# Optimization experiments

Measured on AMD Instinct MI355X. Metric: run time of the kernel, lower is better.

Reference implementation:

```python
import math
import jax, jax.numpy as jnp
import numpy as np

B, T, D, N = 4, 4096, 2048, 512
FACIL_RATE = 2.0
FIRE_THRESH = 0.85
MAX_GATE = 8.0
EPS = 1e-12  # F.normalize eps


def _gelu(x):
    c = math.sqrt(2.0 / math.pi)
    return 0.5 * x * (1.0 + jnp.tanh(c * (x + 0.044715 * x ** 3)))


def _normalize(v, axis=-1):
    n = jnp.linalg.norm(v, axis=axis, keepdims=True)
    return v / jnp.maximum(n, EPS)


def setup_inputs() -> dict:
    key = jax.random.key(0)
    k1, k2, k3 = jax.random.split(key, 3)
    return {
        "x": jax.random.normal(k1, (B, T, D), dtype=jnp.float32),
        "log_k_mag": jnp.asarray(math.log(0.5), dtype=jnp.float32),
        "keys": jax.random.normal(k2, (N, D), dtype=jnp.float32),
        "mag": jax.random.uniform(k3, (N, D), dtype=jnp.float32, minval=0.1, maxval=1.0),
        "facil": jnp.full((N,), 2.0, dtype=jnp.float32),
        "mask": jnp.ones((N,), dtype=bool),
    }


def reference(x, log_k_mag, keys, mag, facil, mask):
    Bb, Tt, Dd = x.shape
    k_mag = jnp.clip(jnp.exp(log_k_mag), 0.01, 5.0)
    y = _gelu(x)  # [B,T,D]
    # torch detaches y before the buffer math
    y_flat = jax.lax.stop_gradient(y.reshape(Bb * Tt, Dd))
    y_mean = y_flat.mean(0)  # [D]
    m_n = _normalize(y_mean, axis=0)
    keys_n = _normalize(keys)  # [N,D]
    sims = jnp.where(mask, keys_n @ m_n, -1.0)  # [N]
    idx = jnp.argmax(sims)
    fire = sims[idx] > FIRE_THRESH
    facil_level = jnp.where(fire, facil[idx] * FACIL_RATE, facil[idx])
    mag_vec = mag[idx]  # [D]
    importance = mag_vec / jnp.maximum(mag_vec.mean(), 1e-6)
    mv_n = keys_n[idx]  # [D] (already L2-normalized key)
    y_n = _normalize(y_flat)  # [B*T, D]
    tok_sim = jnp.clip(y_n @ mv_n, 0.0, 1.0).reshape(Bb, Tt, 1)
    gate_d = jnp.minimum(1.0 + k_mag * (facil_level - 1.0) * importance, MAX_GATE)  # [D]
    gate = gate_d.reshape(1, 1, Dd) * tok_sim + (1.0 - tok_sim)
    return y * gate
```

## Files before the change

kernel.cpp:

```cpp
#include <hip/hip_runtime.h>
#include <math.h>

#define ROWS 16384
#define D    2048
#define NKEYS 512
#define NCHUNK 1024
#define CROWS (ROWS / NCHUNK)
#define NPANEL 8
#define PCOLS (D / NPANEL)

__device__ inline float gelu1(float v) {
    float t = 0.7978845608028654f * fmaf(0.044715f * v, v * v, v);
    float e = __expf(2.0f * t);
    return v * (1.0f - 1.0f / (e + 1.0f));
}

__device__ inline float4 gelu4(float4 v) {
    float4 r;
    r.x = gelu1(v.x); r.y = gelu1(v.y); r.z = gelu1(v.z); r.w = gelu1(v.w);
    return r;
}

__device__ inline void acc4(float4& a, float4 v) {
    a.x += v.x; a.y += v.y; a.z += v.z; a.w += v.w;
}

__device__ inline void block_reduce_sum2(float& a, float& b) {
    __shared__ float sa[4], sb[4];
    for (int off = 32; off; off >>= 1) {
        a += __shfl_down(a, off, 64);
        b += __shfl_down(b, off, 64);
    }
    const int lane = threadIdx.x & 63, w = threadIdx.x >> 6;
    if (lane == 0) { sa[w] = a; sb[w] = b; }
    __syncthreads();
    if (threadIdx.x == 0) {
        a = sa[0] + sa[1] + sa[2] + sa[3];
        b = sb[0] + sb[1] + sb[2] + sb[3];
        sa[0] = a; sb[0] = b;
    }
    __syncthreads();
    a = sa[0]; b = sb[0];
    __syncthreads();
}

__global__ __launch_bounds__(256) void colsum_kernel(const float* __restrict__ x,
                                                     float* __restrict__ partials) {
    const int rc = blockIdx.x >> 3;
    const int p  = blockIdx.x & 7;
    const int t  = threadIdx.x;
    const int w    = t >> 6;
    const int lane = t & 63;

    const size_t base = (size_t)(rc * CROWS + w) * (D / 4) + p * (PCOLS / 4) + lane;
    const float4* x4 = (const float4*)x;
    float4 l0 = x4[base + 0 * 4 * (D / 4)];
    float4 l1 = x4[base + 1 * 4 * (D / 4)];
    float4 l2 = x4[base + 2 * 4 * (D / 4)];
    float4 l3 = x4[base + 3 * 4 * (D / 4)];

    float4 a = gelu4(l0);
    acc4(a, gelu4(l1));
    acc4(a, gelu4(l2));
    acc4(a, gelu4(l3));

    __shared__ float4 sm[4][64];
    sm[w][lane] = a;
    __syncthreads();
    if (t < 64) {
        float4 s = sm[0][t];
        acc4(s, sm[1][t]);
        acc4(s, sm[2][t]);
        acc4(s, sm[3][t]);
        float4* pr = (float4*)(partials + (size_t)rc * D + p * PCOLS);
        pr[t] = s;
    }
}

__global__ __launch_bounds__(256) void reduce_kernel(const float* __restrict__ partials,
                                                     float* __restrict__ colsum) {
    const int t = threadIdx.x;
    const int cidx = t & 15;
    const int rg   = t >> 4;
    const int c = blockIdx.x * 16 + cidx;
    float s = 0.f;
    #pragma unroll 8
    for (int r = rg; r < NCHUNK; r += 16) {
        s += partials[(size_t)r * D + c];
    }
    __shared__ float sm[256];
    sm[t] = s;
    __syncthreads();
    if (t < 16) {
        float acc = 0.f;
        #pragma unroll
        for (int k = 0; k < 16; ++k) acc += sm[t + 16 * k];
        colsum[blockIdx.x * 16 + t] = acc;
    }
}

__global__ __launch_bounds__(256) void sims_kernel(const float* __restrict__ keys,
                                                   const float* __restrict__ colsum,
                                                   float* __restrict__ sims) {
    const int i = blockIdx.x;
    const int t = threadIdx.x;
    const float4* kr = (const float4*)(keys + (size_t)i * D);
    const float4* s4 = (const float4*)colsum;
    float4 k0 = kr[t], k1 = kr[t + 256];
    float4 c0 = s4[t], c1 = s4[t + 256];
    float dot = k0.x*c0.x + k0.y*c0.y + k0.z*c0.z + k0.w*c0.w
              + k1.x*c1.x + k1.y*c1.y + k1.z*c1.z + k1.w*c1.w;
    float ksq = k0.x*k0.x + k0.y*k0.y + k0.z*k0.z + k0.w*k0.w
              + k1.x*k1.x + k1.y*k1.y + k1.z*k1.z + k1.w*k1.w;
    block_reduce_sum2(dot, ksq);
    if (t == 0) sims[i] = dot / fmaxf(sqrtf(ksq), 1e-12f);
}

__global__ __launch_bounds__(256) void finalize_kernel(const float* __restrict__ colsum,
                                                       const float* __restrict__ sims,
                                                       const float* __restrict__ keys,
                                                       const float* __restrict__ mag,
                                                       const float* __restrict__ facil,
                                                       const float* __restrict__ logk,
                                                       float* __restrict__ gate_d,
                                                       float* __restrict__ mv_n) {
    const int t = threadIdx.x;
    __shared__ float sv[256];
    __shared__ int   si[256];
    __shared__ int   s_idx;
    __shared__ float s_val;

    float best = -3.402823466e38f; int bidx = 0;
    for (int i = t; i < NKEYS; i += 256) {
        float v = sims[i];
        if (v > best) { best = v; bidx = i; }
    }
    sv[t] = best; si[t] = bidx;
    __syncthreads();
    if (t == 0) {
        float bv = sv[0]; int bi = si[0];
        for (int i = 1; i < 256; i++) {
            if (sv[i] > bv || (sv[i] == bv && si[i] < bi)) { bv = sv[i]; bi = si[i]; }
        }
        s_idx = bi; s_val = bv;
    }
    __syncthreads();
    const int idx = s_idx;

    float ss = 0.f, dummy = 0.f;
    for (int d = t; d < D; d += 256) { float v = colsum[d]; ss += v * v; }
    block_reduce_sum2(ss, dummy);
    const float normS = fmaxf(sqrtf(ss), 1e-12f);
    const float true_sim = s_val / normS;
    const bool fire = true_sim > 0.85f;

    const float fl = facil[idx] * (fire ? 2.0f : 1.0f);
    const float km = fminf(fmaxf(expf(logk[0]), 0.01f), 5.0f);

    const float4* mrow4 = (const float4*)(mag  + (size_t)idx * D);
    const float4* krow4 = (const float4*)(keys + (size_t)idx * D);
    float4 mA = mrow4[t], mB = mrow4[t + 256];
    float4 kA = krow4[t], kB = krow4[t + 256];
    float msum = mA.x + mA.y + mA.z + mA.w + mB.x + mB.y + mB.z + mB.w;
    float ksq  = kA.x*kA.x + kA.y*kA.y + kA.z*kA.z + kA.w*kA.w
               + kB.x*kB.x + kB.y*kB.y + kB.z*kB.z + kB.w*kB.w;
    block_reduce_sum2(msum, ksq);
    const float mmean = fmaxf(msum / (float)D, 1e-6f);
    const float knorm = fmaxf(sqrtf(ksq), 1e-12f);
    const float coef = km * (fl - 1.0f) / mmean;
    const float rkn = 1.0f / knorm;

    float4 gA, gB, nA, nB;
    gA.x = fminf(fmaf(coef, mA.x, 1.0f), 8.0f);
    gA.y = fminf(fmaf(coef, mA.y, 1.0f), 8.0f);
    gA.z = fminf(fmaf(coef, mA.z, 1.0f), 8.0f);
    gA.w = fminf(fmaf(coef, mA.w, 1.0f), 8.0f);
    gB.x = fminf(fmaf(coef, mB.x, 1.0f), 8.0f);
    gB.y = fminf(fmaf(coef, mB.y, 1.0f), 8.0f);
    gB.z = fminf(fmaf(coef, mB.z, 1.0f), 8.0f);
    gB.w = fminf(fmaf(coef, mB.w, 1.0f), 8.0f);
    nA.x = kA.x * rkn; nA.y = kA.y * rkn; nA.z = kA.z * rkn; nA.w = kA.w * rkn;
    nB.x = kB.x * rkn; nB.y = kB.y * rkn; nB.z = kB.z * rkn; nB.w = kB.w * rkn;

    float4* g4 = (float4*)gate_d;
    float4* n4 = (float4*)mv_n;
    g4[t]       = gA;
    g4[t + 256] = gB;
    n4[t]       = nA;
    n4[t + 256] = nB;
}

__global__ __launch_bounds__(256) void main_kernel(const float* __restrict__ x,
                                                   const float* __restrict__ gate_d,
                                                   const float* __restrict__ mv_n,
                                                   float* __restrict__ out) {
    const int w    = threadIdx.x >> 6;
    const int lane = threadIdx.x & 63;
    const int row  = blockIdx.x * 4 + w;

    const float4* xr  = (const float4*)(x + (size_t)row * D) + lane;
    const float4* mv4 = (const float4*)mv_n + lane;

    float4 xv[8];
    #pragma unroll
    for (int i = 0; i < 8; ++i) xv[i] = xr[i * 64];

    float4 y[8];
    float dot = 0.f, ss = 0.f;
    #pragma unroll
    for (int i = 0; i < 8; ++i) {
        y[i] = gelu4(xv[i]);
        float4 m = mv4[i * 64];
        dot += y[i].x*m.x + y[i].y*m.y + y[i].z*m.z + y[i].w*m.w;
        ss  += y[i].x*y[i].x + y[i].y*y[i].y + y[i].z*y[i].z + y[i].w*y[i].w;
    }

    #pragma unroll
    for (int off = 32; off; off >>= 1) {
        dot += __shfl_xor(dot, off, 64);
        ss  += __shfl_xor(ss,  off, 64);
    }

    float ts = dot / fmaxf(sqrtf(ss), 1e-12f);
    ts = fminf(fmaxf(ts, 0.0f), 1.0f);
    const float omts = 1.0f - ts;

    const float4* g4 = (const float4*)gate_d + lane;
    float4* o4 = (float4*)(out + (size_t)row * D) + lane;
    #pragma unroll
    for (int i = 0; i < 8; ++i) {
        float4 g = g4[i * 64];
        float4 o;
        o.x = y[i].x * fmaf(g.x, ts, omts);
        o.y = y[i].y * fmaf(g.y, ts, omts);
        o.z = y[i].z * fmaf(g.z, ts, omts);
        o.w = y[i].w * fmaf(g.w, ts, omts);
        o4[i * 64] = o;
    }
}

extern "C" void kernel_launch(void* const* d_in, const int* in_sizes, int n_in,
                              void* d_out, int out_size, void* d_ws, size_t ws_size,
                              hipStream_t stream) {
    const float* x     = (const float*)d_in[0];
    const float* logk  = (const float*)d_in[1];
    const float* keys  = (const float*)d_in[2];
    const float* mag   = (const float*)d_in[3];
    const float* facil = (const float*)d_in[4];
    float* out = (float*)d_out;

    float* ws       = (float*)d_ws;
    float* colsum   = ws;
    float* sims     = ws + 2048;
    float* gate_d   = ws + 2560;
    float* mv_n     = ws + 4608;
    float* partials = ws + 6656;

    colsum_kernel  <<<NCHUNK * NPANEL, 256, 0, stream>>>(x, partials);
    reduce_kernel  <<<D / 16, 256, 0, stream>>>(partials, colsum);
    sims_kernel    <<<NKEYS, 256, 0, stream>>>(keys, colsum, sims);
    finalize_kernel<<<1, 256, 0, stream>>>(colsum, sims, keys, mag, facil, logk, gate_d, mv_n);
    main_kernel    <<<ROWS / 4, 256, 0, stream>>>(x, gate_d, mv_n, out);
}
```

Baseline: 104.2 us.

## Cache GELU output as fp16 in first pass and reuse it in apply

The first pass now computes GELU once, writes it as fp16 to workspace, and accumulates column partials over 16-row blocks. The apply kernel reads the fp16 activations instead of recomputing GELU from fp32 input, and uses nontemporal loads and stores. This trades a full fp32 re-read plus GELU recompute for an fp16 write and read, at the cost of output precision.

```diff
diff --git a/kernel.cpp b/kernel.cpp
--- a/kernel.cpp
+++ b/kernel.cpp
@@ -5,9 +5,10 @@
 #define D    2048
 #define NKEYS 512
 #define NCHUNK 1024
-#define CROWS (ROWS / NCHUNK)
-#define NPANEL 8
-#define PCOLS (D / NPANEL)
+
+typedef float    fvec4 __attribute__((ext_vector_type(4)));
+typedef _Float16 half4 __attribute__((ext_vector_type(4)));
+typedef _Float16 half8 __attribute__((ext_vector_type(8)));
 
 __device__ inline float gelu1(float v) {
     float t = 0.7978845608028654f * fmaf(0.044715f * v, v * v, v);
@@ -16,6 +17,11 @@
 }
 
 __device__ inline float4 gelu4(float4 v) {
+    float4 r;
+    r.x = gelu1(v.x); r.y = gelu1(v.y); r.z = gelu1(v.z); r.w = gelu1(v.w);
+    return r;
+}
+__device__ inline float4 gelu4(fvec4 v) {
     float4 r;
     r.x = gelu1(v.x); r.y = gelu1(v.y); r.z = gelu1(v.z); r.w = gelu1(v.w);
     return r;
@@ -44,37 +50,51 @@
     __syncthreads();
 }
 
-__global__ __launch_bounds__(256) void colsum_kernel(const float* __restrict__ x,
-                                                     float* __restrict__ partials) {
-    const int rc = blockIdx.x >> 3;
-    const int p  = blockIdx.x & 7;
-    const int t  = threadIdx.x;
-    const int w    = t >> 6;
-    const int lane = t & 63;
-
-    const size_t base = (size_t)(rc * CROWS + w) * (D / 4) + p * (PCOLS / 4) + lane;
-    const float4* x4 = (const float4*)x;
-    float4 l0 = x4[base + 0 * 4 * (D / 4)];
-    float4 l1 = x4[base + 1 * 4 * (D / 4)];
-    float4 l2 = x4[base + 2 * 4 * (D / 4)];
-    float4 l3 = x4[base + 3 * 4 * (D / 4)];
-
-    float4 a = gelu4(l0);
-    acc4(a, gelu4(l1));
-    acc4(a, gelu4(l2));
-    acc4(a, gelu4(l3));
-
-    __shared__ float4 sm[4][64];
-    sm[w][lane] = a;
-    __syncthreads();
-    if (t < 64) {
-        float4 s = sm[0][t];
-        acc4(s, sm[1][t]);
-        acc4(s, sm[2][t]);
-        acc4(s, sm[3][t]);
-        float4* pr = (float4*)(partials + (size_t)rc * D + p * PCOLS);
-        pr[t] = s;
-    }
+__global__ __launch_bounds__(256) void pass1_kernel(const float* __restrict__ x,
+                                                    _Float16* __restrict__ yh,
+                                                    float* __restrict__ partials) {
+    const int b = blockIdx.x;
+    const int t = threadIdx.x;
+    const int w = t >> 6, lane = t & 63;
+
+    float4 acc[8];
+    #pragma unroll
+    for (int i = 0; i < 8; ++i) acc[i] = float4{0.f, 0.f, 0.f, 0.f};
+
+    #pragma unroll
+    for (int j = 0; j < 4; ++j) {
+        const int row = b * 16 + w * 4 + j;
+        const fvec4* xr = (const fvec4*)(x + (size_t)row * D) + lane;
+        fvec4 v[8];
+        #pragma unroll
+        for (int i = 0; i < 8; ++i) v[i] = __builtin_nontemporal_load(&xr[i * 64]);
+        _Float16* yr = yh + (size_t)row * D + lane * 4;
+        #pragma unroll
+        for (int i = 0; i < 8; ++i) {
+            float4 y = gelu4(v[i]);
+            acc4(acc[i], y);
+            half4 h;
+            h.x = (_Float16)y.x; h.y = (_Float16)y.y;
+            h.z = (_Float16)y.z; h.w = (_Float16)y.w;
+            *(half4*)(yr + i * 256) = h;
+        }
+    }
+
+    __shared__ float4 sm[4][64][9];
+    #pragma unroll
+    for (int i = 0; i < 8; ++i) sm[w][lane][i] = acc[i];
+    __syncthreads();
+    const int i0 = t >> 5;
+    const int l0 = (t & 31) * 2;
+    float4 s0 = float4{0.f,0.f,0.f,0.f}, s1 = float4{0.f,0.f,0.f,0.f};
+    #pragma unroll
+    for (int ww = 0; ww < 4; ++ww) {
+        acc4(s0, sm[ww][l0][i0]);
+        acc4(s1, sm[ww][l0 + 1][i0]);
+    }
+    float4* pr = (float4*)(partials + (size_t)b * D + t * 8);
+    pr[0] = s0;
+    pr[1] = s1;
 }
 
 __global__ __launch_bounds__(256) void reduce_kernel(const float* __restrict__ partials,
@@ -190,29 +210,34 @@
     n4[t + 256] = nB;
 }
 
-__global__ __launch_bounds__(256) void main_kernel(const float* __restrict__ x,
-                                                   const float* __restrict__ gate_d,
-                                                   const float* __restrict__ mv_n,
-                                                   float* __restrict__ out) {
+__global__ __launch_bounds__(256) void apply_kernel(const _Float16* __restrict__ yh,
+                                                    const float* __restrict__ gate_d,
+                                                    const float* __restrict__ mv_n,
+                                                    float* __restrict__ out) {
     const int w    = threadIdx.x >> 6;
     const int lane = threadIdx.x & 63;
     const int row  = blockIdx.x * 4 + w;
 
-    const float4* xr  = (const float4*)(x + (size_t)row * D) + lane;
-    const float4* mv4 = (const float4*)mv_n + lane;
-
-    float4 xv[8];
-    #pragma unroll
-    for (int i = 0; i < 8; ++i) xv[i] = xr[i * 64];
-
-    float4 y[8];
+    const half8* yr = (const half8*)(yh + (size_t)row * D) + lane;
+    float yv[32];
+    #pragma unroll
+    for (int k = 0; k < 4; ++k) {
+        half8 h = __builtin_nontemporal_load(&yr[k * 64]);
+        #pragma unroll
+        for (int e = 0; e < 8; ++e) yv[k * 8 + e] = (float)h[e];
+    }
+
+    const float4* mv4 = (const float4*)mv_n;
     float dot = 0.f, ss = 0.f;
     #pragma unroll
-    for (int i = 0; i < 8; ++i) {
-        y[i] = gelu4(xv[i]);
-        float4 m = mv4[i * 64];
-        dot += y[i].x*m.x + y[i].y*m.y + y[i].z*m.z + y[i].w*m.w;
-        ss  += y[i].x*y[i].x + y[i].y*y[i].y + y[i].z*y[i].z + y[i].w*y[i].w;
+    for (int k = 0; k < 4; ++k) {
+        float4 m0 = mv4[k * 128 + lane * 2];
+        float4 m1 = mv4[k * 128 + lane * 2 + 1];
+        const float* yb = &yv[k * 8];
+        dot += yb[0]*m0.x + yb[1]*m0.y + yb[2]*m0.z + yb[3]*m0.w
+             + yb[4]*m1.x + yb[5]*m1.y + yb[6]*m1.z + yb[7]*m1.w;
+        ss  += yb[0]*yb[0] + yb[1]*yb[1] + yb[2]*yb[2] + yb[3]*yb[3]
+             + yb[4]*yb[4] + yb[5]*yb[5] + yb[6]*yb[6] + yb[7]*yb[7];
     }
 
     #pragma unroll
@@ -225,17 +250,24 @@
     ts = fminf(fmaxf(ts, 0.0f), 1.0f);
     const float omts = 1.0f - ts;
 
-    const float4* g4 = (const float4*)gate_d + lane;
-    float4* o4 = (float4*)(out + (size_t)row * D) + lane;
-    #pragma unroll
-    for (int i = 0; i < 8; ++i) {
-        float4 g = g4[i * 64];
-        float4 o;
-        o.x = y[i].x * fmaf(g.x, ts, omts);
-        o.y = y[i].y * fmaf(g.y, ts, omts);
-        o.z = y[i].z * fmaf(g.z, ts, omts);
-        o.w = y[i].w * fmaf(g.w, ts, omts);
-        o4[i * 64] = o;
+    const float4* g4 = (const float4*)gate_d;
+    fvec4* o4 = (fvec4*)(out + (size_t)row * D);
+    #pragma unroll
+    for (int k = 0; k < 4; ++k) {
+        float4 g0 = g4[k * 128 + lane * 2];
+        float4 g1 = g4[k * 128 + lane * 2 + 1];
+        const float* yb = &yv[k * 8];
+        fvec4 o0, o1;
+        o0.x = yb[0] * fmaf(g0.x, ts, omts);
+        o0.y = yb[1] * fmaf(g0.y, ts, omts);
+        o0.z = yb[2] * fmaf(g0.z, ts, omts);
+        o0.w = yb[3] * fmaf(g0.w, ts, omts);
+        o1.x = yb[4] * fmaf(g1.x, ts, omts);
+        o1.y = yb[5] * fmaf(g1.y, ts, omts);
+        o1.z = yb[6] * fmaf(g1.z, ts, omts);
+        o1.w = yb[7] * fmaf(g1.w, ts, omts);
+        __builtin_nontemporal_store(o0, &o4[k * 128 + lane * 2]);
+        __builtin_nontemporal_store(o1, &o4[k * 128 + lane * 2 + 1]);
     }
 }
 
@@ -255,10 +287,11 @@
     float* gate_d   = ws + 2560;
     float* mv_n     = ws + 4608;
     float* partials = ws + 6656;
-
-    colsum_kernel  <<<NCHUNK * NPANEL, 256, 0, stream>>>(x, partials);
+    _Float16* yh    = (_Float16*)(ws + 4u * 1024 * 1024);
+
+    pass1_kernel   <<<NCHUNK, 256, 0, stream>>>(x, yh, partials);
     reduce_kernel  <<<D / 16, 256, 0, stream>>>(partials, colsum);
     sims_kernel    <<<NKEYS, 256, 0, stream>>>(keys, colsum, sims);
     finalize_kernel<<<1, 256, 0, stream>>>(colsum, sims, keys, mag, facil, logk, gate_d, mv_n);
-    main_kernel    <<<ROWS / 4, 256, 0, stream>>>(x, gate_d, mv_n, out);
-}
+    apply_kernel   <<<ROWS / 4, 256, 0, stream>>>(yh, gate_d, mv_n, out);
+}
```

After: 142.3 us. +36.5%, slower.
